# Performance work log

Hardware: AMD Instinct MI355X
Metric: run time of the kernel (lower is better)

Reference implementation:

```python
import jax, jax.numpy as jnp
import numpy as np


def setup_inputs() -> dict:
    key = jax.random.key(0)
    k1, k2, k3, k4, k5 = jax.random.split(key, 5)
    B, T, C = 64, 1024, 768
    scale = 1.0 / np.sqrt(C)
    tokens = jax.random.normal(k1, (B, T, C), dtype=jnp.float32)
    mask_topk = jax.random.randint(k2, (B, T), 0, 2) > 0
    Wq = jax.random.normal(k3, (C, C), dtype=jnp.float32) * scale
    Wk = jax.random.normal(k4, (C, C), dtype=jnp.float32) * scale
    Wv = jax.random.normal(k5, (C, C), dtype=jnp.float32) * scale
    return {"tokens": tokens, "mask_topk": mask_topk, "Wq": Wq, "Wk": Wk, "Wv": Wv}


def reference(tokens, mask_topk, Wq, Wk, Wv):
    # tokens: [B, T, C]; mask_topk: [B, T] bool; W*: [C, C] (torch Linear weight, y = x @ W.T)
    C = tokens.shape[-1]
    m = mask_topk.astype(tokens.dtype)                      # [B, T]
    cnt = jnp.sum(m, axis=-1, keepdims=True)                # [B, 1]
    masked_sum = jnp.einsum('btc,bt->bc', tokens, m)        # [B, C]
    mean_all = jnp.mean(tokens, axis=1)                     # fallback when mask is empty
    q_sal = jnp.where(cnt > 0, masked_sum / jnp.maximum(cnt, 1.0), mean_all)  # [B, C]
    q_sal = q_sal[:, None, :]                               # [B, 1, C]

    Q = jnp.einsum('bqc,dc->bqd', q_sal, Wq)                # [B, 1, C]
    K = jnp.einsum('btc,dc->btd', tokens, Wk)               # [B, T, C]
    V = jnp.einsum('btc,dc->btd', tokens, Wv)               # [B, T, C]

    scores = jnp.einsum('bqd,btd->bqt', Q, K) / jnp.sqrt(jnp.asarray(C, tokens.dtype))
    attn = jax.nn.softmax(scores, axis=-1)                  # [B, 1, T]
    v_fg = jnp.einsum('bqt,btd->bqd', attn, V)[:, 0, :]     # [B, C]
    return (v_fg, attn)
```

## Files before the change

kernel.cpp:

```cpp
#include <hip/hip_runtime.h>
#include <hip/hip_bf16.h>

#define B 64
#define T 1024
#define C 768
#define TSPLIT 8
#define TCHUNK (T / TSPLIT)

#define OFF_MSUM   64
#define OFF_ASUM   (OFF_MSUM + B*TSPLIT*C)
#define OFF_QSAL   (OFF_ASUM + B*TSPLIT*C)
#define OFF_Q      (OFF_QSAL + B*C)
#define OFF_QK     (OFF_Q + B*C)
#define OFF_SCORES (OFF_QK + B*C)
#define OFF_PPART  (OFF_SCORES + B*T)
#define OFF_POOLED (OFF_PPART + B*TSPLIT*C)

__device__ __forceinline__ bool read_mask(const void* mask, int mode, int idx) {
    if (mode == 1) return ((const unsigned char*)mask)[idx] != 0;
    if (mode == 2) return ((const float*)mask)[idx] != 0.0f;
    return ((const int*)mask)[idx] != 0;
}

__global__ void k_detect(const void* mask, int* mode_out) {
    __shared__ int s_not01, s_isf;
    int tid = threadIdx.x;
    if (tid == 0) { s_not01 = 0; s_isf = 0; }
    __syncthreads();
    const int* mi = (const int*)mask;
    int not01 = 0, isf = 0;
    for (int k = 0; k < 64; ++k) {
        int v = mi[tid + 256 * k];
        if (v != 0 && v != 1) not01 = 1;
        if (v == 0x3F800000) isf = 1;
    }
    if (not01) atomicOr(&s_not01, 1);
    if (isf)   atomicOr(&s_isf, 1);
    __syncthreads();
    if (tid == 0) *mode_out = s_isf ? 2 : (s_not01 ? 1 : 0);
}

__global__ void k_partial_sums(const float* __restrict__ tokens, const void* mask,
                               const int* modep, float* __restrict__ msum,
                               float* __restrict__ asum) {
    int ts = blockIdx.x, b = blockIdx.y, tid = threadIdx.x;
    int mode = *modep;
    int c = tid * 4;
    float4 ms = {0, 0, 0, 0}, as = {0, 0, 0, 0};
    const float* tb = tokens + (size_t)b * T * C;
    for (int t = ts * TCHUNK; t < ts * TCHUNK + TCHUNK; ++t) {
        float4 x = *(const float4*)(tb + (size_t)t * C + c);
        as.x += x.x; as.y += x.y; as.z += x.z; as.w += x.w;
        if (read_mask(mask, mode, b * T + t)) {
            ms.x += x.x; ms.y += x.y; ms.z += x.z; ms.w += x.w;
        }
    }
    size_t o = (size_t)(b * TSPLIT + ts) * C + c;
    *(float4*)(msum + o) = ms;
    *(float4*)(asum + o) = as;
}

__global__ void k_qsal(const void* mask, const int* modep,
                       const float* __restrict__ msum, const float* __restrict__ asum,
                       float* __restrict__ qsal) {
    int b = blockIdx.x, tid = threadIdx.x;
    int mode = *modep;
    __shared__ float red[256];
    float cnt0 = 0.f;
    for (int t = tid; t < T; t += 256)
        cnt0 += read_mask(mask, mode, b * T + t) ? 1.f : 0.f;
    red[tid] = cnt0;
    __syncthreads();
    for (int s = 128; s > 0; s >>= 1) {
        if (tid < s) red[tid] += red[tid + s];
        __syncthreads();
    }
    float cnt = red[0];
    float scale = (cnt > 0.f) ? (1.f / fmaxf(cnt, 1.f)) : (1.f / (float)T);
    bool use_masked = (cnt > 0.f);
    for (int c = tid; c < C; c += 256) {
        float m = 0.f, a = 0.f;
        for (int p = 0; p < TSPLIT; ++p) {
            m += msum[(size_t)(b * TSPLIT + p) * C + c];
            a += asum[(size_t)(b * TSPLIT + p) * C + c];
        }
        qsal[b * C + c] = (use_masked ? m : a) * scale;
    }
}

__global__ void k_rowdot(const float* __restrict__ vin, const float* __restrict__ W,
                         float* __restrict__ vout, float scale) {
    int gid = blockIdx.x * 256 + threadIdx.x;
    int b = gid / C, d = gid - b * C;
    const float4* v = (const float4*)(vin + (size_t)b * C);
    const float4* w = (const float4*)(W + (size_t)d * C);
    float acc = 0.f;
#pragma unroll 4
    for (int j = 0; j < C / 4; ++j) {
        float4 a = v[j], x = w[j];
        acc += a.x * x.x + a.y * x.y + a.z * x.z + a.w * x.w;
    }
    vout[gid] = acc * scale;
}

__global__ void k_coldot(const float* __restrict__ Q, const float* __restrict__ Wk,
                         float* __restrict__ qk) {
    int gid = blockIdx.x * 256 + threadIdx.x;
    int b = gid / C, c = gid - b * C;
    const float* Qb = Q + (size_t)b * C;
    float acc = 0.f;
#pragma unroll 8
    for (int d = 0; d < C; ++d)
        acc += Qb[d] * Wk[(size_t)d * C + c];
    qk[gid] = acc * 0.03608439182435161f;
}

__global__ void k_scores(const float* __restrict__ tokens, const float* __restrict__ qk,
                         float* __restrict__ scores) {
    __shared__ float sq[C];
    int ts = blockIdx.x, b = blockIdx.y, tid = threadIdx.x;
    for (int c = tid; c < C; c += 256) sq[c] = qk[b * C + c];
    __syncthreads();
    int wave = tid >> 6, lane = tid & 63;
    const float* tb = tokens + (size_t)b * T * C;
    for (int i = 0; i < TCHUNK / 4; ++i) {
        int t = ts * TCHUNK + wave * (TCHUNK / 4) + i;
        const float4* row = (const float4*)(tb + (size_t)t * C);
        const float4* q4 = (const float4*)sq;
        float acc = 0.f;
#pragma unroll
        for (int j = 0; j < 3; ++j) {
            int idx = lane + 64 * j;
            float4 x = row[idx], q = q4[idx];
            acc += x.x * q.x + x.y * q.y + x.z * q.z + x.w * q.w;
        }
        for (int s = 32; s > 0; s >>= 1) acc += __shfl_xor(acc, s);
        if (lane == 0) scores[b * T + t] = acc;
    }
}

__global__ void k_softmax(const float* __restrict__ scores, float* __restrict__ attn) {
    int b = blockIdx.x, tid = threadIdx.x;
    __shared__ float red[256];
    float4 s4 = ((const float4*)(scores + (size_t)b * T))[tid];
    float mx = fmaxf(fmaxf(s4.x, s4.y), fmaxf(s4.z, s4.w));
    red[tid] = mx;
    __syncthreads();
    for (int s = 128; s > 0; s >>= 1) {
        if (tid < s) red[tid] = fmaxf(red[tid], red[tid + s]);
        __syncthreads();
    }
    mx = red[0];
    __syncthreads();
    float4 e;
    e.x = expf(s4.x - mx); e.y = expf(s4.y - mx);
    e.z = expf(s4.z - mx); e.w = expf(s4.w - mx);
    red[tid] = e.x + e.y + e.z + e.w;
    __syncthreads();
    for (int s = 128; s > 0; s >>= 1) {
        if (tid < s) red[tid] += red[tid + s];
        __syncthreads();
    }
    float inv = 1.f / red[0];
    float4 o = {e.x * inv, e.y * inv, e.z * inv, e.w * inv};
    ((float4*)(attn + (size_t)b * T))[tid] = o;
}

__global__ void k_pool_partial(const float* __restrict__ tokens, const float* __restrict__ attn,
                               float* __restrict__ ppart) {
    int ts = blockIdx.x, b = blockIdx.y, tid = threadIdx.x;
    int c = tid * 4;
    float4 acc = {0, 0, 0, 0};
    const float* tb = tokens + (size_t)b * T * C;
    for (int t = ts * TCHUNK; t < ts * TCHUNK + TCHUNK; ++t) {
        float a = attn[(size_t)b * T + t];
        float4 x = *(const float4*)(tb + (size_t)t * C + c);
        acc.x += a * x.x; acc.y += a * x.y; acc.z += a * x.z; acc.w += a * x.w;
    }
    *(float4*)(ppart + (size_t)(b * TSPLIT + ts) * C + c) = acc;
}

__global__ void k_pool_reduce(const float* __restrict__ ppart, float* __restrict__ pooled) {
    int gid = blockIdx.x * 256 + threadIdx.x;
    int b = gid / C, c = gid - b * C;
    float a = 0.f;
#pragma unroll
    for (int p = 0; p < TSPLIT; ++p)
        a += ppart[(size_t)(b * TSPLIT + p) * C + c];
    pooled[gid] = a;
}

extern "C" void kernel_launch(void* const* d_in, const int* in_sizes, int n_in,
                              void* d_out, int out_size, void* d_ws, size_t ws_size,
                              hipStream_t stream) {
    const float* tokens = (const float*)d_in[0];
    const void*  mask   = d_in[1];
    const float* Wq     = (const float*)d_in[2];
    const float* Wk     = (const float*)d_in[3];
    const float* Wv     = (const float*)d_in[4];

    float* ws     = (float*)d_ws;
    int*   mode   = (int*)d_ws;
    float* msum   = ws + OFF_MSUM;
    float* asum   = ws + OFF_ASUM;
    float* qsal   = ws + OFF_QSAL;
    float* Qv     = ws + OFF_Q;
    float* qk     = ws + OFF_QK;
    float* scores = ws + OFF_SCORES;
    float* ppart  = ws + OFF_PPART;
    float* pooled = ws + OFF_POOLED;

    float* v_fg = (float*)d_out;
    float* attn = (float*)d_out + B * C;

    k_detect<<<1, 256, 0, stream>>>(mask, mode);
    k_partial_sums<<<dim3(TSPLIT, B), 192, 0, stream>>>(tokens, mask, mode, msum, asum);
    k_qsal<<<B, 256, 0, stream>>>(mask, mode, msum, asum, qsal);
    k_rowdot<<<(B * C) / 256, 256, 0, stream>>>(qsal, Wq, Qv, 1.0f);
    k_coldot<<<(B * C) / 256, 256, 0, stream>>>(Qv, Wk, qk);
    k_scores<<<dim3(TSPLIT, B), 256, 0, stream>>>(tokens, qk, scores);
    k_softmax<<<B, 256, 0, stream>>>(scores, attn);
    k_pool_partial<<<dim3(TSPLIT, B), 192, 0, stream>>>(tokens, attn, ppart);
    k_pool_reduce<<<(B * C) / 256, 256, 0, stream>>>(ppart, pooled);
    k_rowdot<<<(B * C) / 256, 256, 0, stream>>>(pooled, Wv, v_fg, 1.0f);
}
```

Measured before the change: 209.2 us.

## Fuse scores, local softmax and pooling with split-softmax combine; raise T split

Merges the score, softmax and attention-weighted pooling passes into one kernel per T-chunk. Each chunk computes local max and exp-sums (flash-decoding style) and the rescaling happens in a small combine kernel and in the pooling reduction. This is meant to cut one full read of tokens and two launches. It also raises TSPLIT from 8 to 32 for more blocks, splits the rowdot/coldot matvecs across 4 threads per output with shuffle reductions, and stages the mask in shared memory for branchless masked sums. The costs are larger partial buffers and a longer reduction over 32 partials.

```diff
diff --git a/kernel.cpp b/kernel.cpp
--- a/kernel.cpp
+++ b/kernel.cpp
@@ -4,7 +4,7 @@
 #define B 64
 #define T 1024
 #define C 768
-#define TSPLIT 8
+#define TSPLIT 32
 #define TCHUNK (T / TSPLIT)
 
 #define OFF_MSUM   64
@@ -13,7 +13,10 @@
 #define OFF_Q      (OFF_QSAL + B*C)
 #define OFF_QK     (OFF_Q + B*C)
 #define OFF_SCORES (OFF_QK + B*C)
-#define OFF_PPART  (OFF_SCORES + B*T)
+#define OFF_MPART  (OFF_SCORES + B*T)
+#define OFF_SPART  (OFF_MPART + B*TSPLIT)
+#define OFF_COEF   (OFF_SPART + B*TSPLIT)
+#define OFF_PPART  (OFF_COEF + B*TSPLIT)
 #define OFF_POOLED (OFF_PPART + B*TSPLIT*C)
 
 __device__ __forceinline__ bool read_mask(const void* mask, int mode, int idx) {
@@ -45,15 +48,20 @@
                                float* __restrict__ asum) {
     int ts = blockIdx.x, b = blockIdx.y, tid = threadIdx.x;
     int mode = *modep;
+    __shared__ float s_m[TCHUNK];
+    if (tid < TCHUNK)
+        s_m[tid] = read_mask(mask, mode, b * T + ts * TCHUNK + tid) ? 1.f : 0.f;
+    __syncthreads();
     int c = tid * 4;
     float4 ms = {0, 0, 0, 0}, as = {0, 0, 0, 0};
     const float* tb = tokens + (size_t)b * T * C;
-    for (int t = ts * TCHUNK; t < ts * TCHUNK + TCHUNK; ++t) {
+#pragma unroll 4
+    for (int r = 0; r < TCHUNK; ++r) {
+        int t = ts * TCHUNK + r;
         float4 x = *(const float4*)(tb + (size_t)t * C + c);
         as.x += x.x; as.y += x.y; as.z += x.z; as.w += x.w;
-        if (read_mask(mask, mode, b * T + t)) {
-            ms.x += x.x; ms.y += x.y; ms.z += x.z; ms.w += x.w;
-        }
+        float wm = s_m[r];
+        ms.x += wm * x.x; ms.y += wm * x.y; ms.z += wm * x.z; ms.w += wm * x.w;
     }
     size_t o = (size_t)(b * TSPLIT + ts) * C + c;
     *(float4*)(msum + o) = ms;
@@ -80,6 +88,7 @@
     bool use_masked = (cnt > 0.f);
     for (int c = tid; c < C; c += 256) {
         float m = 0.f, a = 0.f;
+#pragma unroll 8
         for (int p = 0; p < TSPLIT; ++p) {
             m += msum[(size_t)(b * TSPLIT + p) * C + c];
             a += asum[(size_t)(b * TSPLIT + p) * C + c];
@@ -88,45 +97,60 @@
     }
 }
 
-__global__ void k_rowdot(const float* __restrict__ vin, const float* __restrict__ W,
-                         float* __restrict__ vout, float scale) {
-    int gid = blockIdx.x * 256 + threadIdx.x;
+__global__ void k_rowdot4(const float* __restrict__ vin, const float* __restrict__ W,
+                          float* __restrict__ vout, float scale) {
+    int tid = threadIdx.x;
+    int gid = blockIdx.x * 64 + (tid >> 2);
+    int sub = tid & 3;
     int b = gid / C, d = gid - b * C;
     const float4* v = (const float4*)(vin + (size_t)b * C);
     const float4* w = (const float4*)(W + (size_t)d * C);
     float acc = 0.f;
-#pragma unroll 4
-    for (int j = 0; j < C / 4; ++j) {
+    int j0 = sub * 48;
+#pragma unroll 8
+    for (int j = j0; j < j0 + 48; ++j) {
         float4 a = v[j], x = w[j];
         acc += a.x * x.x + a.y * x.y + a.z * x.z + a.w * x.w;
     }
-    vout[gid] = acc * scale;
-}
-
-__global__ void k_coldot(const float* __restrict__ Q, const float* __restrict__ Wk,
-                         float* __restrict__ qk) {
-    int gid = blockIdx.x * 256 + threadIdx.x;
+    acc += __shfl_xor(acc, 1);
+    acc += __shfl_xor(acc, 2);
+    if (sub == 0) vout[gid] = acc * scale;
+}
+
+__global__ void k_coldot4(const float* __restrict__ Q, const float* __restrict__ Wk,
+                          float* __restrict__ qk) {
+    int tid = threadIdx.x;
+    int gid = blockIdx.x * 64 + (tid >> 2);
+    int sub = tid & 3;
     int b = gid / C, c = gid - b * C;
     const float* Qb = Q + (size_t)b * C;
     float acc = 0.f;
-#pragma unroll 8
-    for (int d = 0; d < C; ++d)
+    int d0 = sub * 192;
+#pragma unroll 8
+    for (int i = 0; i < 192; ++i) {
+        int d = d0 + i;
         acc += Qb[d] * Wk[(size_t)d * C + c];
-    qk[gid] = acc * 0.03608439182435161f;
-}
-
-__global__ void k_scores(const float* __restrict__ tokens, const float* __restrict__ qk,
-                         float* __restrict__ scores) {
+    }
+    acc += __shfl_xor(acc, 1);
+    acc += __shfl_xor(acc, 2);
+    if (sub == 0) qk[gid] = acc * 0.03608439182435161f;
+}
+
+__global__ void k_fused(const float* __restrict__ tokens, const float* __restrict__ qk,
+                        float* __restrict__ scores, float* __restrict__ mpart,
+                        float* __restrict__ spart, float* __restrict__ ppart) {
     __shared__ float sq[C];
+    __shared__ float ssc[TCHUNK];
+    __shared__ float sw[TCHUNK];
     int ts = blockIdx.x, b = blockIdx.y, tid = threadIdx.x;
-    for (int c = tid; c < C; c += 256) sq[c] = qk[b * C + c];
+    ((float4*)sq)[tid] = ((const float4*)(qk + (size_t)b * C))[tid];
     __syncthreads();
     int wave = tid >> 6, lane = tid & 63;
     const float* tb = tokens + (size_t)b * T * C;
-    for (int i = 0; i < TCHUNK / 4; ++i) {
-        int t = ts * TCHUNK + wave * (TCHUNK / 4) + i;
+    const float4* q4 = (const float4*)sq;
+    for (int r = wave; r < TCHUNK; r += 3) {
+        int t = ts * TCHUNK + r;
         const float4* row = (const float4*)(tb + (size_t)t * C);
-        const float4* q4 = (const float4*)sq;
         float acc = 0.f;
 #pragma unroll
         for (int j = 0; j < 3; ++j) {
@@ -135,58 +159,60 @@
             acc += x.x * q.x + x.y * q.y + x.z * q.z + x.w * q.w;
         }
         for (int s = 32; s > 0; s >>= 1) acc += __shfl_xor(acc, s);
-        if (lane == 0) scores[b * T + t] = acc;
-    }
-}
-
-__global__ void k_softmax(const float* __restrict__ scores, float* __restrict__ attn) {
-    int b = blockIdx.x, tid = threadIdx.x;
-    __shared__ float red[256];
-    float4 s4 = ((const float4*)(scores + (size_t)b * T))[tid];
-    float mx = fmaxf(fmaxf(s4.x, s4.y), fmaxf(s4.z, s4.w));
-    red[tid] = mx;
-    __syncthreads();
-    for (int s = 128; s > 0; s >>= 1) {
-        if (tid < s) red[tid] = fmaxf(red[tid], red[tid + s]);
-        __syncthreads();
-    }
-    mx = red[0];
-    __syncthreads();
-    float4 e;
-    e.x = expf(s4.x - mx); e.y = expf(s4.y - mx);
-    e.z = expf(s4.z - mx); e.w = expf(s4.w - mx);
-    red[tid] = e.x + e.y + e.z + e.w;
-    __syncthreads();
-    for (int s = 128; s > 0; s >>= 1) {
-        if (tid < s) red[tid] += red[tid + s];
-        __syncthreads();
-    }
-    float inv = 1.f / red[0];
-    float4 o = {e.x * inv, e.y * inv, e.z * inv, e.w * inv};
-    ((float4*)(attn + (size_t)b * T))[tid] = o;
-}
-
-__global__ void k_pool_partial(const float* __restrict__ tokens, const float* __restrict__ attn,
-                               float* __restrict__ ppart) {
-    int ts = blockIdx.x, b = blockIdx.y, tid = threadIdx.x;
+        if (lane == 0) { ssc[r] = acc; scores[(size_t)b * T + t] = acc; }
+    }
+    __syncthreads();
+    float m = -3.4e38f;
+#pragma unroll
+    for (int r = 0; r < TCHUNK; ++r) m = fmaxf(m, ssc[r]);
+    if (tid < TCHUNK) sw[tid] = expf(ssc[tid] - m);
+    __syncthreads();
+    float s = 0.f;
+#pragma unroll
+    for (int r = 0; r < TCHUNK; ++r) s += sw[r];
     int c = tid * 4;
     float4 acc = {0, 0, 0, 0};
-    const float* tb = tokens + (size_t)b * T * C;
-    for (int t = ts * TCHUNK; t < ts * TCHUNK + TCHUNK; ++t) {
-        float a = attn[(size_t)b * T + t];
+#pragma unroll 4
+    for (int r = 0; r < TCHUNK; ++r) {
+        int t = ts * TCHUNK + r;
+        float wv = sw[r];
         float4 x = *(const float4*)(tb + (size_t)t * C + c);
-        acc.x += a * x.x; acc.y += a * x.y; acc.z += a * x.z; acc.w += a * x.w;
+        acc.x += wv * x.x; acc.y += wv * x.y; acc.z += wv * x.z; acc.w += wv * x.w;
     }
     *(float4*)(ppart + (size_t)(b * TSPLIT + ts) * C + c) = acc;
-}
-
-__global__ void k_pool_reduce(const float* __restrict__ ppart, float* __restrict__ pooled) {
+    if (tid == 0) { mpart[b * TSPLIT + ts] = m; spart[b * TSPLIT + ts] = s; }
+}
+
+__global__ void k_combine(const float* __restrict__ scores, const float* __restrict__ mpart,
+                          const float* __restrict__ spart, float* __restrict__ coef,
+                          float* __restrict__ attn) {
+    int b = blockIdx.x, tid = threadIdx.x;
+    __shared__ float sm[TSPLIT], ss[TSPLIT];
+    if (tid < TSPLIT) { sm[tid] = mpart[b * TSPLIT + tid]; ss[tid] = spart[b * TSPLIT + tid]; }
+    __syncthreads();
+    float M = -3.4e38f;
+#pragma unroll
+    for (int p = 0; p < TSPLIT; ++p) M = fmaxf(M, sm[p]);
+    float Z = 0.f;
+#pragma unroll
+    for (int p = 0; p < TSPLIT; ++p) Z += ss[p] * expf(sm[p] - M);
+    float invZ = 1.f / Z;
+    if (tid < TSPLIT) coef[b * TSPLIT + tid] = expf(sm[tid] - M) * invZ;
+    float4 sc = ((const float4*)(scores + (size_t)b * T))[tid];
+    float4 o;
+    o.x = expf(sc.x - M) * invZ; o.y = expf(sc.y - M) * invZ;
+    o.z = expf(sc.z - M) * invZ; o.w = expf(sc.w - M) * invZ;
+    ((float4*)(attn + (size_t)b * T))[tid] = o;
+}
+
+__global__ void k_pool_reduce(const float* __restrict__ ppart, const float* __restrict__ coef,
+                              float* __restrict__ pooled) {
     int gid = blockIdx.x * 256 + threadIdx.x;
     int b = gid / C, c = gid - b * C;
     float a = 0.f;
-#pragma unroll
+#pragma unroll 8
     for (int p = 0; p < TSPLIT; ++p)
-        a += ppart[(size_t)(b * TSPLIT + p) * C + c];
+        a += coef[b * TSPLIT + p] * ppart[(size_t)(b * TSPLIT + p) * C + c];
     pooled[gid] = a;
 }
 
@@ -207,6 +233,9 @@
     float* Qv     = ws + OFF_Q;
     float* qk     = ws + OFF_QK;
     float* scores = ws + OFF_SCORES;
+    float* mpart  = ws + OFF_MPART;
+    float* spart  = ws + OFF_SPART;
+    float* coef   = ws + OFF_COEF;
     float* ppart  = ws + OFF_PPART;
     float* pooled = ws + OFF_POOLED;
 
@@ -216,11 +245,10 @@
     k_detect<<<1, 256, 0, stream>>>(mask, mode);
     k_partial_sums<<<dim3(TSPLIT, B), 192, 0, stream>>>(tokens, mask, mode, msum, asum);
     k_qsal<<<B, 256, 0, stream>>>(mask, mode, msum, asum, qsal);
-    k_rowdot<<<(B * C) / 256, 256, 0, stream>>>(qsal, Wq, Qv, 1.0f);
-    k_coldot<<<(B * C) / 256, 256, 0, stream>>>(Qv, Wk, qk);
-    k_scores<<<dim3(TSPLIT, B), 256, 0, stream>>>(tokens, qk, scores);
-    k_softmax<<<B, 256, 0, stream>>>(scores, attn);
-    k_pool_partial<<<dim3(TSPLIT, B), 192, 0, stream>>>(tokens, attn, ppart);
-    k_pool_reduce<<<(B * C) / 256, 256, 0, stream>>>(ppart, pooled);
-    k_rowdot<<<(B * C) / 256, 256, 0, stream>>>(pooled, Wv, v_fg, 1.0f);
-}
+    k_rowdot4<<<(B * C) / 64, 256, 0, stream>>>(qsal, Wq, Qv, 1.0f);
+    k_coldot4<<<(B * C) / 64, 256, 0, stream>>>(Qv, Wk, qk);
+    k_fused<<<dim3(TSPLIT, B), 192, 0, stream>>>(tokens, qk, scores, mpart, spart, ppart);
+    k_combine<<<B, 256, 0, stream>>>(scores, mpart, spart, coef, attn);
+    k_pool_reduce<<<(B * C) / 256, 256, 0, stream>>>(ppart, coef, pooled);
+    k_rowdot4<<<(B * C) / 64, 256, 0, stream>>>(pooled, Wv, v_fg, 1.0f);
+}
```

After: 214.0 us. 2.3% more time.
